# Kernel optimization log

Measured on AMD Instinct MI355X. Metric: run time of the kernel, lower is better.

## Reference

```python
import jax, jax.numpy as jnp
import numpy as np

D_MODEL = 1024
NUM_HEADS = 16
HEAD_DIM = D_MODEL // NUM_HEADS
SCALE = HEAD_DIM ** -0.5


def setup_inputs() -> dict:
    key = jax.random.key(0)
    ks = jax.random.split(key, 8)
    B, Nq, Nk = 2, 2048, 2048
    s = D_MODEL ** -0.5  # init scale for weights
    return {
        "query": jax.random.normal(ks[0], (B, Nq, D_MODEL), jnp.float32),
        "key": jax.random.normal(ks[1], (B, Nk, D_MODEL), jnp.float32),
        "value": jax.random.normal(ks[2], (B, Nk, D_MODEL), jnp.float32),
        "Wq": jax.random.normal(ks[3], (D_MODEL, D_MODEL), jnp.float32) * s,
        "Wk": jax.random.normal(ks[4], (D_MODEL, D_MODEL), jnp.float32) * s,
        "Wv": jax.random.normal(ks[5], (D_MODEL, D_MODEL), jnp.float32) * s,
        "Wo": jax.random.normal(ks[6], (D_MODEL, D_MODEL), jnp.float32) * s,
        "bo": jnp.zeros((D_MODEL,), jnp.float32),
    }


def reference(query, key, value, Wq, Wk, Wv, Wo, bo):
    B, Nq, C = query.shape
    Nk = key.shape[1]
    H, Dh = NUM_HEADS, HEAD_DIM
    # projections (torch Linear: x @ W.T)
    q = (query @ Wq.T).reshape(B, Nq, H, Dh).transpose(0, 2, 1, 3)  # [B,H,Nq,Dh]
    k = (key @ Wk.T).reshape(B, Nk, H, Dh).transpose(0, 2, 1, 3)    # [B,H,Nk,Dh]
    v = (value @ Wv.T).reshape(B, Nk, H, Dh).transpose(0, 2, 1, 3)  # [B,H,Nk,Dh]
    # explicit attention: QK^T * scale -> softmax -> @V
    sim = jnp.einsum("bhqd,bhkd->bhqk", q, k) * SCALE
    attn = jax.nn.softmax(sim, axis=-1)
    out = jnp.einsum("bhqk,bhkd->bhqd", attn, v)
    out = out.transpose(0, 2, 1, 3).reshape(B, Nq, C)
    return out @ Wo.T + bo
```

## Files before the change

kernel.cpp:

```cpp
#include <hip/hip_runtime.h>
#include <hip/hip_bf16.h>

typedef __attribute__((ext_vector_type(8))) short short8;
typedef __attribute__((ext_vector_type(4))) short short4v;
typedef __attribute__((ext_vector_type(4))) float f32x4;

#define DEVFN static __device__ __forceinline__

constexpr int D_MODEL = 1024;
constexpr int NH  = 16;
constexpr int DH  = 64;
constexpr int SEQ = 2048;
constexpr float SCALE_LOG2E = 0.125f * 1.44269504088896341f;

DEVFN short bf16s(float f) {
  __hip_bfloat16 h = __float2bfloat16(f);
  short s; __builtin_memcpy(&s, &h, 2);
  return s;
}

DEVFN float fast_exp2(float x) {
#if __has_builtin(__builtin_amdgcn_exp2f)
  return __builtin_amdgcn_exp2f(x);
#else
  return exp2f(x);
#endif
}

DEVFN int inc3(int x) { return x == 2 ? 0 : x + 1; }

DEVFN void gload_lds16(const void* g, void* l) {
  __builtin_amdgcn_global_load_lds(
      (const __attribute__((address_space(1))) unsigned int*)g,
      (__attribute__((address_space(3))) unsigned int*)l, 16, 0, 0);
}

__global__ __launch_bounds__(256)
void castk(const float* __restrict__ src, short* __restrict__ dst, int n8, float scale)
{
  int i = blockIdx.x * blockDim.x + threadIdx.x;
  if (i >= n8) return;
  const float4 a = *(const float4*)(src + (size_t)i*8);
  const float4 b = *(const float4*)(src + (size_t)i*8 + 4);
  short8 v;
  v[0]=bf16s(a.x*scale); v[1]=bf16s(a.y*scale); v[2]=bf16s(a.z*scale); v[3]=bf16s(a.w*scale);
  v[4]=bf16s(b.x*scale); v[5]=bf16s(b.y*scale); v[6]=bf16s(b.z*scale); v[7]=bf16s(b.w*scale);
  *(short8*)(dst + (size_t)i*8) = v;
}

__global__ __launch_bounds__(256, 2)
void qkv_gemm(const float* __restrict__ Aq, const float* __restrict__ Ak,
              const float* __restrict__ Av,
              const short* __restrict__ Wq, const short* __restrict__ Wk,
              const short* __restrict__ Wv,
              short* __restrict__ Qp, short* __restrict__ Kp, short* __restrict__ Vp)
{
  __shared__ char smem[3*24576];

  const int id  = blockIdx.x;
  const int swz = (id & 7)*96 + (id >> 3);
  const int z   = swz >> 8;
  const int rr  = swz & 255;
  const int m0  = (rr >> 3) * 128, n0 = (rr & 7) * 128;

  const float* Af = (z == 0) ? Aq : (z == 1) ? Ak : Av;
  const short* Wb = (z == 0) ? Wq : (z == 1) ? Wk : Wv;
  short* Cp       = (z == 0) ? Qp : (z == 1) ? Kp : Vp;

  const int tid = threadIdx.x, lane = tid & 63, w = tid >> 6;
  const int wr = w >> 1, wc = w & 1;
  const int l15 = lane & 15, l4 = lane >> 4;

  f32x4 acc[4][4];
  #pragma unroll
  for (int i = 0; i < 4; ++i)
    #pragma unroll
    for (int j = 0; j < 4; ++j) acc[i][j] = f32x4{0.f,0.f,0.f,0.f};

  auto stage = [&](int sb, int k0) {
    char* buf = smem + sb*24576;
    #pragma unroll
    for (int p = 0; p < 4; ++p) {
      const int off = (w*4 + p)*1024 + lane*16;
      const int row = off >> 7;
      const int cb  = (off & 127) ^ ((row & 7) << 4);
      gload_lds16(Af + (size_t)(m0 + row)*D_MODEL + k0 + (cb >> 2),
                  buf + (w*4 + p)*1024);
    }
    #pragma unroll
    for (int p = 0; p < 2; ++p) {
      const int off = (w*2 + p)*1024 + lane*16;
      const int row = off >> 6;
      const int cb  = (off & 63) ^ ((row & 3) << 4);
      gload_lds16(Wb + (size_t)(n0 + row)*D_MODEL + k0 + (cb >> 1),
                  buf + 16384 + (w*2 + p)*1024);
    }
  };

  auto compute = [&](int cb_) {
    char* AsB = smem + cb_*24576;
    char* WsB = AsB + 16384;
    short8 af[4], bf[4];
    #pragma unroll
    for (int fi = 0; fi < 4; ++fi) {
      const int row = wr*64 + fi*16 + l15;
      const int s_ = (row & 7) << 4;
      f32x4 x0 = *(const f32x4*)(AsB + row*128 + ((l4*32) ^ s_));
      f32x4 x1 = *(const f32x4*)(AsB + row*128 + ((l4*32 + 16) ^ s_));
      short8 a;
      a[0]=bf16s(x0[0]); a[1]=bf16s(x0[1]); a[2]=bf16s(x0[2]); a[3]=bf16s(x0[3]);
      a[4]=bf16s(x1[0]); a[5]=bf16s(x1[1]); a[6]=bf16s(x1[2]); a[7]=bf16s(x1[3]);
      af[fi] = a;
    }
    #pragma unroll
    for (int fj = 0; fj < 4; ++fj) {
      const int row = wc*64 + fj*16 + l15;
      bf[fj] = *(const short8*)(WsB + row*64 + ((l4*16) ^ ((row & 3) << 4)));
    }
    #pragma unroll
    for (int fi = 0; fi < 4; ++fi)
      #pragma unroll
      for (int fj = 0; fj < 4; ++fj)
        acc[fi][fj] = __builtin_amdgcn_mfma_f32_16x16x32_bf16(af[fi], bf[fj], acc[fi][fj], 0, 0, 0);
  };

  constexpr int NIT = D_MODEL/32;
  stage(0, 0);
  stage(1, 32);
  int cur = 0, nxt = 2;
  for (int kt = 0; kt < NIT-1; ++kt) {
    asm volatile("s_waitcnt vmcnt(6)" ::: "memory");
    __builtin_amdgcn_s_barrier();
    __builtin_amdgcn_sched_barrier(0);
    if (kt + 2 < NIT) stage(nxt, (kt+2)*32);
    compute(cur);
    cur = inc3(cur); nxt = inc3(nxt);
  }
  asm volatile("s_waitcnt vmcnt(0)" ::: "memory");
  __builtin_amdgcn_s_barrier();
  __builtin_amdgcn_sched_barrier(0);
  compute(cur);

  #pragma unroll
  for (int fi = 0; fi < 4; ++fi)
    #pragma unroll
    for (int fj = 0; fj < 4; ++fj)
      #pragma unroll
      for (int r = 0; r < 4; ++r) {
        const int m = m0 + wr*64 + fi*16 + l4*4 + r;
        const int j = n0 + wc*64 + fj*16 + l15;
        const int b = m >> 11, n = m & (SEQ-1);
        const int h = j >> 6,  d = j & 63;
        const short v = bf16s(acc[fi][fj][r]);
        if (z == 2)
          Cp[((size_t)(b*NH + h)*DH + d)*SEQ + n] = v;
        else
          Cp[(((size_t)(b*NH + h)*SEQ + n) << 6) + d] = v;
      }
}

__global__ __launch_bounds__(256, 4)
void gemm_out(const short* __restrict__ A, const short* __restrict__ Wb,
              const float* __restrict__ bias, float* __restrict__ Cp)
{
  __shared__ char smem[3*12288];

  const int id  = blockIdx.x;
  const int swz = (id & 7)*64 + (id >> 3);
  const int m0  = (swz >> 4) * 128, n0 = (swz & 15) * 64;

  const int tid = threadIdx.x, lane = tid & 63, w = tid >> 6;
  const int wr = w >> 1, wc = w & 1;
  const int l15 = lane & 15, l4 = lane >> 4;

  f32x4 acc[4][2];
  #pragma unroll
  for (int i = 0; i < 4; ++i)
    #pragma unroll
    for (int j = 0; j < 2; ++j) acc[i][j] = f32x4{0.f,0.f,0.f,0.f};

  auto stage = [&](int sb, int k0) {
    char* buf = smem + sb*12288;
    #pragma unroll
    for (int p = 0; p < 2; ++p) {
      const int off = (w*2 + p)*1024 + lane*16;
      const int row = off >> 6;
      const int cb  = (off & 63) ^ ((row & 3) << 4);
      gload_lds16(A + (size_t)(m0 + row)*D_MODEL + k0 + (cb >> 1),
                  buf + (w*2 + p)*1024);
    }
    {
      const int off = w*1024 + lane*16;
      const int row = off >> 6;
      const int cb  = (off & 63) ^ ((row & 3) << 4);
      gload_lds16(Wb + (size_t)(n0 + row)*D_MODEL + k0 + (cb >> 1),
                  buf + 8192 + w*1024);
    }
  };

  auto compute = [&](int cb_) {
    char* AsB = smem + cb_*12288;
    char* WsB = AsB + 8192;
    short8 af[4], bf[2];
    #pragma unroll
    for (int fi = 0; fi < 4; ++fi) {
      const int row = wr*64 + fi*16 + l15;
      af[fi] = *(const short8*)(AsB + row*64 + ((l4*16) ^ ((row & 3) << 4)));
    }
    #pragma unroll
    for (int fj = 0; fj < 2; ++fj) {
      const int row = wc*32 + fj*16 + l15;
      bf[fj] = *(const short8*)(WsB + row*64 + ((l4*16) ^ ((row & 3) << 4)));
    }
    #pragma unroll
    for (int fi = 0; fi < 4; ++fi)
      #pragma unroll
      for (int fj = 0; fj < 2; ++fj)
        acc[fi][fj] = __builtin_amdgcn_mfma_f32_16x16x32_bf16(af[fi], bf[fj], acc[fi][fj], 0, 0, 0);
  };

  constexpr int NIT = D_MODEL/32;
  stage(0, 0);
  stage(1, 32);
  int cur = 0, nxt = 2;
  for (int kt = 0; kt < NIT-1; ++kt) {
    asm volatile("s_waitcnt vmcnt(3)" ::: "memory");
    __builtin_amdgcn_s_barrier();
    __builtin_amdgcn_sched_barrier(0);
    if (kt + 2 < NIT) stage(nxt, (kt+2)*32);
    compute(cur);
    cur = inc3(cur); nxt = inc3(nxt);
  }
  asm volatile("s_waitcnt vmcnt(0)" ::: "memory");
  __builtin_amdgcn_s_barrier();
  __builtin_amdgcn_sched_barrier(0);
  compute(cur);

  float bj[2];
  #pragma unroll
  for (int fj = 0; fj < 2; ++fj) bj[fj] = bias[n0 + wc*32 + fj*16 + l15];
  #pragma unroll
  for (int fi = 0; fi < 4; ++fi)
    #pragma unroll
    for (int fj = 0; fj < 2; ++fj)
      #pragma unroll
      for (int r = 0; r < 4; ++r) {
        const int m = m0 + wr*64 + fi*16 + l4*4 + r;
        const int j = n0 + wc*32 + fj*16 + l15;
        Cp[(size_t)m*D_MODEL + j] = acc[fi][fj][r] + bj[fj];
      }
}

__global__ __launch_bounds__(512, 4)
void attn_fwd(const short* __restrict__ Qh, const short* __restrict__ Kh,
              const short* __restrict__ Vt, __hip_bfloat16* __restrict__ AO)
{
  __shared__ char smem[3*16384 + 16384];
  char* PsAll = smem + 49152;

  const int id  = blockIdx.x;
  const int swz = (id & 7)*64 + (id >> 3);
  const int bh  = swz >> 4;
  const int q0  = (swz & 15) * 128;

  const int tid = threadIdx.x, lane = tid & 63, w = tid >> 6;
  const int l15 = lane & 15, l4 = lane >> 4;
  const int b = bh >> 4, h = bh & 15;
  const size_t base = (size_t)bh * SEQ * DH;
  char* PsB = PsAll + w * 2048;

  const short* Kg = Kh + base;
  const short* Vg = Vt + base;

  short8 qf[2];
  #pragma unroll
  for (int kc = 0; kc < 2; ++kc)
    qf[kc] = *(const short8*)(Qh + base + (size_t)(q0 + w*16 + l15)*DH + kc*32 + l4*8);

  float m = -1e30f, l = 0.f;
  f32x4 o[4];
  #pragma unroll
  for (int fj = 0; fj < 4; ++fj) o[fj] = f32x4{0.f,0.f,0.f,0.f};

  const int soff = w*1024 + lane*16;
  const int srow = soff >> 7;
  const int scb  = (soff & 127) ^ ((srow & 7) << 4);

  auto stage = [&](int sb, int kt) {
    char* buf = smem + sb*16384;
    gload_lds16(Kg + (size_t)(kt*64 + srow)*DH + (scb >> 1), buf + w*1024);
    gload_lds16(Vg + (size_t)srow*SEQ + kt*64 + (scb >> 1),  buf + 8192 + w*1024);
  };

  auto compute = [&](int cb_) {
    char* KsB = smem + cb_*16384;
    char* VsB = KsB + 8192;

    f32x4 s[4];
    #pragma unroll
    for (int fj = 0; fj < 4; ++fj) s[fj] = f32x4{0.f,0.f,0.f,0.f};
    #pragma unroll
    for (int kc = 0; kc < 2; ++kc)
      #pragma unroll
      for (int fj = 0; fj < 4; ++fj) {
        const int row = fj*16 + l15;
        short8 kf = *(const short8*)(KsB + ((row*128 + (kc*32 + l4*8)*2) ^ ((row & 7) << 4)));
        s[fj] = __builtin_amdgcn_mfma_f32_16x16x32_bf16(kf, qf[kc], s[fj], 0, 0, 0);
      }

    float pmax = s[0][0];
    #pragma unroll
    for (int fj = 0; fj < 4; ++fj)
      #pragma unroll
      for (int r = 0; r < 4; ++r) pmax = fmaxf(pmax, s[fj][r]);
    pmax = fmaxf(pmax, __shfl_xor(pmax, 16, 64));
    pmax = fmaxf(pmax, __shfl_xor(pmax, 32, 64));

    if (!__all(pmax <= m)) {
      const float mn = fmaxf(m, pmax);
      const float al = fast_exp2(m - mn);
      m = mn;
      l *= al;
      float alr[4];
      #pragma unroll
      for (int r = 0; r < 4; ++r) alr[r] = __shfl(al, l4*4 + r, 64);
      #pragma unroll
      for (int fj = 0; fj < 4; ++fj)
        #pragma unroll
        for (int r = 0; r < 4; ++r) o[fj][r] *= alr[r];
    }

    float rs = 0.f;
    #pragma unroll
    for (int fj = 0; fj < 4; ++fj)
      #pragma unroll
      for (int r = 0; r < 4; ++r) {
        s[fj][r] = fast_exp2(s[fj][r] - m);
        rs += s[fj][r];
      }
    rs += __shfl_xor(rs, 16, 64);
    rs += __shfl_xor(rs, 32, 64);
    l += rs;

    #pragma unroll
    for (int fj = 0; fj < 4; ++fj) {
      short4v c;
      c[0]=bf16s(s[fj][0]); c[1]=bf16s(s[fj][1]); c[2]=bf16s(s[fj][2]); c[3]=bf16s(s[fj][3]);
      const int byo = (l15*128 + (fj*16 + l4*4)*2) ^ ((l15 & 7) << 4);
      *(short4v*)(PsB + byo) = c;
    }

    #pragma unroll
    for (int kc = 0; kc < 2; ++kc) {
      const int pb = (l15*128 + (kc*32 + l4*8)*2) ^ ((l15 & 7) << 4);
      short8 pa = *(const short8*)(PsB + pb);
      #pragma unroll
      for (int fj = 0; fj < 4; ++fj) {
        const int row = fj*16 + l15;
        short8 vf = *(const short8*)(VsB + ((row*128 + (kc*32 + l4*8)*2) ^ ((row & 7) << 4)));
        o[fj] = __builtin_amdgcn_mfma_f32_16x16x32_bf16(pa, vf, o[fj], 0, 0, 0);
      }
    }
  };

  constexpr int NT = SEQ/64;
  stage(0, 0);
  stage(1, 1);
  int cur = 0, nxt = 2;
  for (int kt = 0; kt < NT-1; ++kt) {
    asm volatile("s_waitcnt vmcnt(2)" ::: "memory");
    __builtin_amdgcn_s_barrier();
    __builtin_amdgcn_sched_barrier(0);
    if (kt + 2 < NT) stage(nxt, kt + 2);
    compute(cur);
    cur = inc3(cur); nxt = inc3(nxt);
  }
  asm volatile("s_waitcnt vmcnt(0)" ::: "memory");
  __builtin_amdgcn_s_barrier();
  __builtin_amdgcn_sched_barrier(0);
  compute(cur);

  const float inv = 1.0f / l;
  float ivr[4];
  #pragma unroll
  for (int r = 0; r < 4; ++r) ivr[r] = __shfl(inv, l4*4 + r, 64);
  #pragma unroll
  for (int fj = 0; fj < 4; ++fj)
    #pragma unroll
    for (int r = 0; r < 4; ++r) {
      const int n = q0 + w*16 + l4*4 + r;
      const int d = h*64 + fj*16 + l15;
      AO[(size_t)(b*SEQ + n)*D_MODEL + d] = __float2bfloat16(o[fj][r] * ivr[r]);
    }
}

extern "C" void kernel_launch(void* const* d_in, const int* in_sizes, int n_in,
                              void* d_out, int out_size, void* d_ws, size_t ws_size,
                              hipStream_t stream)
{
  const float* query = (const float*)d_in[0];
  const float* key_  = (const float*)d_in[1];
  const float* value = (const float*)d_in[2];
  const float* Wq = (const float*)d_in[3];
  const float* Wk = (const float*)d_in[4];
  const float* Wv = (const float*)d_in[5];
  const float* Wo = (const float*)d_in[6];
  const float* bo = (const float*)d_in[7];

  char* wsb = (char*)d_ws;
  short* Qp  = (short*)(wsb);
  short* Kp  = (short*)(wsb + (8u  << 20));
  short* Vp  = (short*)(wsb + (16u << 20));
  short* Wqb = (short*)(wsb + (24u << 20));
  short* Wkb = (short*)(wsb + (26u << 20));
  short* Wvb = (short*)(wsb + (28u << 20));
  short* Ao  = (short*)(wsb + (24u << 20));
  short* Wob = (short*)(wsb);

  const int nW = D_MODEL*D_MODEL/8;
  castk<<<nW/256, 256, 0, stream>>>(Wq, Wqb, nW, SCALE_LOG2E);
  castk<<<nW/256, 256, 0, stream>>>(Wk, Wkb, nW, 1.f);
  castk<<<nW/256, 256, 0, stream>>>(Wv, Wvb, nW, 1.f);

  qkv_gemm<<<768, 256, 0, stream>>>(query, key_, value, Wqb, Wkb, Wvb, Qp, Kp, Vp);
  attn_fwd<<<512, 512, 0, stream>>>(Qp, Kp, Vp, (__hip_bfloat16*)Ao);

  castk<<<nW/256, 256, 0, stream>>>(Wo, Wob, nW, 1.f);
  gemm_out<<<512, 256, 0, stream>>>(Ao, Wob, bo, (float*)d_out);
}
```

Before: 238.3 us.

## Pre-cast activations to bf16 and use a unified templated 128x128x64 GEMM

```diff
diff --git a/kernel.cpp b/kernel.cpp
--- a/kernel.cpp
+++ b/kernel.cpp
@@ -48,24 +48,16 @@
   *(short8*)(dst + (size_t)i*8) = v;
 }
 
-__global__ __launch_bounds__(256, 2)
-void qkv_gemm(const float* __restrict__ Aq, const float* __restrict__ Ak,
-              const float* __restrict__ Av,
-              const short* __restrict__ Wq, const short* __restrict__ Wk,
-              const short* __restrict__ Wv,
-              short* __restrict__ Qp, short* __restrict__ Kp, short* __restrict__ Vp)
+template<int MODE>
+__global__ __launch_bounds__(256, 1)
+void gemm_bf(const short* __restrict__ A, const short* __restrict__ W,
+             const float* __restrict__ bias, void* __restrict__ Cp)
 {
-  __shared__ char smem[3*24576];
+  __shared__ char smem[3*32768];
 
   const int id  = blockIdx.x;
-  const int swz = (id & 7)*96 + (id >> 3);
-  const int z   = swz >> 8;
-  const int rr  = swz & 255;
-  const int m0  = (rr >> 3) * 128, n0 = (rr & 7) * 128;
-
-  const float* Af = (z == 0) ? Aq : (z == 1) ? Ak : Av;
-  const short* Wb = (z == 0) ? Wq : (z == 1) ? Wk : Wv;
-  short* Cp       = (z == 0) ? Qp : (z == 1) ? Kp : Vp;
+  const int swz = (id & 7)*32 + (id >> 3);
+  const int m0  = (swz >> 3) * 128, n0 = (swz & 7) * 128;
 
   const int tid = threadIdx.x, lane = tid & 63, w = tid >> 6;
   const int wr = w >> 1, wc = w & 1;
@@ -77,62 +69,66 @@
     #pragma unroll
     for (int j = 0; j < 4; ++j) acc[i][j] = f32x4{0.f,0.f,0.f,0.f};
 
-  auto stage = [&](int sb, int k0) {
-    char* buf = smem + sb*24576;
+  auto stage = [&](int sb, int kt) {
+    char* buf = smem + sb*32768;
     #pragma unroll
     for (int p = 0; p < 4; ++p) {
       const int off = (w*4 + p)*1024 + lane*16;
       const int row = off >> 7;
       const int cb  = (off & 127) ^ ((row & 7) << 4);
-      gload_lds16(Af + (size_t)(m0 + row)*D_MODEL + k0 + (cb >> 2),
-                  buf + (w*4 + p)*1024);
-    }
-    #pragma unroll
-    for (int p = 0; p < 2; ++p) {
-      const int off = (w*2 + p)*1024 + lane*16;
-      const int row = off >> 6;
-      const int cb  = (off & 63) ^ ((row & 3) << 4);
-      gload_lds16(Wb + (size_t)(n0 + row)*D_MODEL + k0 + (cb >> 1),
-                  buf + 16384 + (w*2 + p)*1024);
+      const short* src;
+      if (MODE == 2) {
+        const int m = m0 + row;
+        const int bb = m >> 11, ss = m & (SEQ-1);
+        src = A + (((size_t)(bb*NH + kt)*SEQ + ss) << 6) + (cb >> 1);
+      } else {
+        src = A + (size_t)(m0 + row)*D_MODEL + kt*64 + (cb >> 1);
+      }
+      gload_lds16(src, buf + (w*4 + p)*1024);
+    }
+    #pragma unroll
+    for (int p = 0; p < 4; ++p) {
+      const int off = (w*4 + p)*1024 + lane*16;
+      const int row = off >> 7;
+      const int cb  = (off & 127) ^ ((row & 7) << 4);
+      gload_lds16(W + (size_t)(n0 + row)*D_MODEL + kt*64 + (cb >> 1),
+                  buf + 16384 + (w*4 + p)*1024);
     }
   };
 
   auto compute = [&](int cb_) {
-    char* AsB = smem + cb_*24576;
+    char* AsB = smem + cb_*32768;
     char* WsB = AsB + 16384;
-    short8 af[4], bf[4];
-    #pragma unroll
-    for (int fi = 0; fi < 4; ++fi) {
-      const int row = wr*64 + fi*16 + l15;
-      const int s_ = (row & 7) << 4;
-      f32x4 x0 = *(const f32x4*)(AsB + row*128 + ((l4*32) ^ s_));
-      f32x4 x1 = *(const f32x4*)(AsB + row*128 + ((l4*32 + 16) ^ s_));
-      short8 a;
-      a[0]=bf16s(x0[0]); a[1]=bf16s(x0[1]); a[2]=bf16s(x0[2]); a[3]=bf16s(x0[3]);
-      a[4]=bf16s(x1[0]); a[5]=bf16s(x1[1]); a[6]=bf16s(x1[2]); a[7]=bf16s(x1[3]);
-      af[fi] = a;
-    }
-    #pragma unroll
-    for (int fj = 0; fj < 4; ++fj) {
-      const int row = wc*64 + fj*16 + l15;
-      bf[fj] = *(const short8*)(WsB + row*64 + ((l4*16) ^ ((row & 3) << 4)));
-    }
-    #pragma unroll
-    for (int fi = 0; fi < 4; ++fi)
-      #pragma unroll
-      for (int fj = 0; fj < 4; ++fj)
-        acc[fi][fj] = __builtin_amdgcn_mfma_f32_16x16x32_bf16(af[fi], bf[fj], acc[fi][fj], 0, 0, 0);
+    #pragma unroll
+    for (int kc = 0; kc < 2; ++kc) {
+      short8 af[4], bf[4];
+      #pragma unroll
+      for (int fi = 0; fi < 4; ++fi) {
+        const int row = wr*64 + fi*16 + l15;
+        af[fi] = *(const short8*)(AsB + row*128 + ((kc*64 + l4*16) ^ ((row & 7) << 4)));
+      }
+      #pragma unroll
+      for (int fj = 0; fj < 4; ++fj) {
+        const int row = wc*64 + fj*16 + l15;
+        bf[fj] = *(const short8*)(WsB + row*128 + ((kc*64 + l4*16) ^ ((row & 7) << 4)));
+      }
+      #pragma unroll
+      for (int fi = 0; fi < 4; ++fi)
+        #pragma unroll
+        for (int fj = 0; fj < 4; ++fj)
+          acc[fi][fj] = __builtin_amdgcn_mfma_f32_16x16x32_bf16(af[fi], bf[fj], acc[fi][fj], 0, 0, 0);
+    }
   };
 
-  constexpr int NIT = D_MODEL/32;
+  constexpr int NIT = D_MODEL/64;
   stage(0, 0);
-  stage(1, 32);
+  stage(1, 1);
   int cur = 0, nxt = 2;
   for (int kt = 0; kt < NIT-1; ++kt) {
-    asm volatile("s_waitcnt vmcnt(6)" ::: "memory");
+    asm volatile("s_waitcnt vmcnt(8)" ::: "memory");
     __builtin_amdgcn_s_barrier();
     __builtin_amdgcn_sched_barrier(0);
-    if (kt + 2 < NIT) stage(nxt, (kt+2)*32);
+    if (kt + 2 < NIT) stage(nxt, kt + 2);
     compute(cur);
     cur = inc3(cur); nxt = inc3(nxt);
   }
@@ -141,119 +137,43 @@
   __builtin_amdgcn_sched_barrier(0);
   compute(cur);
 
-  #pragma unroll
-  for (int fi = 0; fi < 4; ++fi)
-    #pragma unroll
-    for (int fj = 0; fj < 4; ++fj)
-      #pragma unroll
-      for (int r = 0; r < 4; ++r) {
-        const int m = m0 + wr*64 + fi*16 + l4*4 + r;
-        const int j = n0 + wc*64 + fj*16 + l15;
-        const int b = m >> 11, n = m & (SEQ-1);
-        const int h = j >> 6,  d = j & 63;
-        const short v = bf16s(acc[fi][fj][r]);
-        if (z == 2)
-          Cp[((size_t)(b*NH + h)*DH + d)*SEQ + n] = v;
-        else
-          Cp[(((size_t)(b*NH + h)*SEQ + n) << 6) + d] = v;
-      }
-}
-
-__global__ __launch_bounds__(256, 4)
-void gemm_out(const short* __restrict__ A, const short* __restrict__ Wb,
-              const float* __restrict__ bias, float* __restrict__ Cp)
-{
-  __shared__ char smem[3*12288];
-
-  const int id  = blockIdx.x;
-  const int swz = (id & 7)*64 + (id >> 3);
-  const int m0  = (swz >> 4) * 128, n0 = (swz & 15) * 64;
-
-  const int tid = threadIdx.x, lane = tid & 63, w = tid >> 6;
-  const int wr = w >> 1, wc = w & 1;
-  const int l15 = lane & 15, l4 = lane >> 4;
-
-  f32x4 acc[4][2];
-  #pragma unroll
-  for (int i = 0; i < 4; ++i)
-    #pragma unroll
-    for (int j = 0; j < 2; ++j) acc[i][j] = f32x4{0.f,0.f,0.f,0.f};
-
-  auto stage = [&](int sb, int k0) {
-    char* buf = smem + sb*12288;
-    #pragma unroll
-    for (int p = 0; p < 2; ++p) {
-      const int off = (w*2 + p)*1024 + lane*16;
-      const int row = off >> 6;
-      const int cb  = (off & 63) ^ ((row & 3) << 4);
-      gload_lds16(A + (size_t)(m0 + row)*D_MODEL + k0 + (cb >> 1),
-                  buf + (w*2 + p)*1024);
-    }
-    {
-      const int off = w*1024 + lane*16;
-      const int row = off >> 6;
-      const int cb  = (off & 63) ^ ((row & 3) << 4);
-      gload_lds16(Wb + (size_t)(n0 + row)*D_MODEL + k0 + (cb >> 1),
-                  buf + 8192 + w*1024);
-    }
-  };
-
-  auto compute = [&](int cb_) {
-    char* AsB = smem + cb_*12288;
-    char* WsB = AsB + 8192;
-    short8 af[4], bf[2];
-    #pragma unroll
-    for (int fi = 0; fi < 4; ++fi) {
-      const int row = wr*64 + fi*16 + l15;
-      af[fi] = *(const short8*)(AsB + row*64 + ((l4*16) ^ ((row & 3) << 4)));
-    }
-    #pragma unroll
-    for (int fj = 0; fj < 2; ++fj) {
-      const int row = wc*32 + fj*16 + l15;
-      bf[fj] = *(const short8*)(WsB + row*64 + ((l4*16) ^ ((row & 3) << 4)));
-    }
+  if (MODE == 2) {
+    float bj[4];
+    #pragma unroll
+    for (int fj = 0; fj < 4; ++fj) bj[fj] = bias[n0 + wc*64 + fj*16 + l15];
     #pragma unroll
     for (int fi = 0; fi < 4; ++fi)
       #pragma unroll
-      for (int fj = 0; fj < 2; ++fj)
-        acc[fi][fj] = __builtin_amdgcn_mfma_f32_16x16x32_bf16(af[fi], bf[fj], acc[fi][fj], 0, 0, 0);
-  };
-
-  constexpr int NIT = D_MODEL/32;
-  stage(0, 0);
-  stage(1, 32);
-  int cur = 0, nxt = 2;
-  for (int kt = 0; kt < NIT-1; ++kt) {
-    asm volatile("s_waitcnt vmcnt(3)" ::: "memory");
-    __builtin_amdgcn_s_barrier();
-    __builtin_amdgcn_sched_barrier(0);
-    if (kt + 2 < NIT) stage(nxt, (kt+2)*32);
-    compute(cur);
-    cur = inc3(cur); nxt = inc3(nxt);
+      for (int fj = 0; fj < 4; ++fj)
+        #pragma unroll
+        for (int r = 0; r < 4; ++r) {
+          const int m = m0 + wr*64 + fi*16 + l4*4 + r;
+          const int j = n0 + wc*64 + fj*16 + l15;
+          ((float*)Cp)[(size_t)m*D_MODEL + j] = acc[fi][fj][r] + bj[fj];
+        }
+  } else {
+    #pragma unroll
+    for (int fi = 0; fi < 4; ++fi)
+      #pragma unroll
+      for (int fj = 0; fj < 4; ++fj)
+        #pragma unroll
+        for (int r = 0; r < 4; ++r) {
+          const int m = m0 + wr*64 + fi*16 + l4*4 + r;
+          const int j = n0 + wc*64 + fj*16 + l15;
+          const int b = m >> 11, n = m & (SEQ-1);
+          const int h = j >> 6,  d = j & 63;
+          const short v = bf16s(acc[fi][fj][r]);
+          if (MODE == 1)
+            ((short*)Cp)[((size_t)(b*NH + h)*DH + d)*SEQ + n] = v;
+          else
+            ((short*)Cp)[(((size_t)(b*NH + h)*SEQ + n) << 6) + d] = v;
+        }
   }
-  asm volatile("s_waitcnt vmcnt(0)" ::: "memory");
-  __builtin_amdgcn_s_barrier();
-  __builtin_amdgcn_sched_barrier(0);
-  compute(cur);
-
-  float bj[2];
-  #pragma unroll
-  for (int fj = 0; fj < 2; ++fj) bj[fj] = bias[n0 + wc*32 + fj*16 + l15];
-  #pragma unroll
-  for (int fi = 0; fi < 4; ++fi)
-    #pragma unroll
-    for (int fj = 0; fj < 2; ++fj)
-      #pragma unroll
-      for (int r = 0; r < 4; ++r) {
-        const int m = m0 + wr*64 + fi*16 + l4*4 + r;
-        const int j = n0 + wc*32 + fj*16 + l15;
-        Cp[(size_t)m*D_MODEL + j] = acc[fi][fj][r] + bj[fj];
-      }
 }
 
 __global__ __launch_bounds__(512, 4)
 void attn_fwd(const short* __restrict__ Qh, const short* __restrict__ Kh,
-              const short* __restrict__ Vt, __hip_bfloat16* __restrict__ AO)
+              const short* __restrict__ Vt, short* __restrict__ AO)
 {
   __shared__ char smem[3*16384 + 16384];
   char* PsAll = smem + 49152;
@@ -389,8 +309,8 @@
     #pragma unroll
     for (int r = 0; r < 4; ++r) {
       const int n = q0 + w*16 + l4*4 + r;
-      const int d = h*64 + fj*16 + l15;
-      AO[(size_t)(b*SEQ + n)*D_MODEL + d] = __float2bfloat16(o[fj][r] * ivr[r]);
+      const int d = fj*16 + l15;
+      AO[(((size_t)(b*NH + h)*SEQ + n) << 6) + d] = bf16s(o[fj][r] * ivr[r]);
     }
 }
 
@@ -408,23 +328,32 @@
   const float* bo = (const float*)d_in[7];
 
   char* wsb = (char*)d_ws;
-  short* Qp  = (short*)(wsb);
-  short* Kp  = (short*)(wsb + (8u  << 20));
-  short* Vp  = (short*)(wsb + (16u << 20));
+  short* Sb  = (short*)(wsb);
+  short* Qp  = (short*)(wsb + (8u  << 20));
+  short* Kp  = (short*)(wsb + (16u << 20));
   short* Wqb = (short*)(wsb + (24u << 20));
   short* Wkb = (short*)(wsb + (26u << 20));
   short* Wvb = (short*)(wsb + (28u << 20));
-  short* Ao  = (short*)(wsb + (24u << 20));
-  short* Wob = (short*)(wsb);
+  short* Wob = (short*)(wsb + (30u << 20));
+  short* Vb  = (short*)d_out;
+  short* Vp  = Sb;
+  short* Ao  = Qp;
 
   const int nW = D_MODEL*D_MODEL/8;
+  const int nI = 4096*D_MODEL/8;
   castk<<<nW/256, 256, 0, stream>>>(Wq, Wqb, nW, SCALE_LOG2E);
   castk<<<nW/256, 256, 0, stream>>>(Wk, Wkb, nW, 1.f);
   castk<<<nW/256, 256, 0, stream>>>(Wv, Wvb, nW, 1.f);
-
-  qkv_gemm<<<768, 256, 0, stream>>>(query, key_, value, Wqb, Wkb, Wvb, Qp, Kp, Vp);
-  attn_fwd<<<512, 512, 0, stream>>>(Qp, Kp, Vp, (__hip_bfloat16*)Ao);
-
   castk<<<nW/256, 256, 0, stream>>>(Wo, Wob, nW, 1.f);
-  gemm_out<<<512, 256, 0, stream>>>(Ao, Wob, bo, (float*)d_out);
-}
+
+  castk<<<nI/256, 256, 0, stream>>>(query, Sb, nI, 1.f);
+  gemm_bf<0><<<256, 256, 0, stream>>>(Sb, Wqb, nullptr, Qp);
+  castk<<<nI/256, 256, 0, stream>>>(key_, Sb, nI, 1.f);
+  gemm_bf<0><<<256, 256, 0, stream>>>(Sb, Wkb, nullptr, Kp);
+  castk<<<nI/256, 256, 0, stream>>>(value, Vb, nI, 1.f);
+  gemm_bf<1><<<256, 256, 0, stream>>>(Vb, Wvb, nullptr, Vp);
+
+  attn_fwd<<<512, 512, 0, stream>>>(Qp, Kp, Vp, Ao);
+
+  gemm_bf<2><<<256, 256, 0, stream>>>(Ao, Wob, bo, d_out);
+}
```

Measured after the change: 237.3 us. Within noise of the previous version (-0.4%).
